# Optimization experiments

Measured on AMD Instinct MI355X. Metric: run time of the kernel, lower is better.

The kernel has to match this reference:

```python
import jax, jax.numpy as jnp
import numpy as np

B, N, K, CIN, COUT, H = 4, 2048, 32, 16, 32, 32
EPS = 1e-5


def setup_inputs() -> dict:
    key = jax.random.key(0)
    ks = jax.random.split(key, 6)
    s = 0.1
    return dict(
        xyz=jax.random.uniform(ks[0], (B, N, 3), dtype=jnp.float32),
        points=jax.random.normal(ks[1], (B, N, CIN), dtype=jnp.float32),
        W1=jax.random.normal(ks[2], (3, H), dtype=jnp.float32) * s,
        b1=jnp.zeros((H,), jnp.float32),
        g1=jnp.ones((H,), jnp.float32),
        be1=jnp.zeros((H,), jnp.float32),
        W2=jax.random.normal(ks[3], (H, H), dtype=jnp.float32) * s,
        b2=jnp.zeros((H,), jnp.float32),
        g2=jnp.ones((H,), jnp.float32),
        be2=jnp.zeros((H,), jnp.float32),
        W3=jax.random.normal(ks[4], (H, CIN * COUT), dtype=jnp.float32) * s,
        b3=jnp.zeros((CIN * COUT,), jnp.float32),
        gbn=jnp.ones((COUT,), jnp.float32),
        bbn=jnp.zeros((COUT,), jnp.float32),
    )


def _bn(h, g, b):
    # BatchNorm1d training-mode math: biased batch stats over axis 0
    return g * (h - h.mean(0)) / jnp.sqrt(h.var(0) + EPS) + b


def reference(xyz, points, W1, b1, g1, be1, W2, b2, g2, be2, W3, b3, gbn, bbn):
    # KNN: squared distances (B,N,N)
    sq = jnp.sum(xyz * xyz, -1)
    dist = -2.0 * jnp.einsum('bmc,bnc->bmn', xyz, xyz) + sq[:, :, None] + sq[:, None, :]
    _, idx = jax.lax.top_k(-dist, K)  # (B,N,K) nearest neighbors

    gather = jax.vmap(lambda p, i: p[i])  # (N,C),(N,K)->(N,K,C), vmapped over B
    grouped_xyz = gather(xyz, idx)                      # (B,N,K,3)
    rel = grouped_xyz - xyz[:, :, None, :]              # (B,N,K,3)
    grouped_pts = gather(points, idx)                   # (B,N,K,CIN)

    # weight net on relative coords
    h = rel.reshape(-1, 3)
    h = _bn(jax.nn.relu(h @ W1 + b1), g1, be1)
    h = _bn(jax.nn.relu(h @ W2 + b2), g2, be2)
    w = (h @ W3 + b3).reshape(B, N, K, CIN, COUT)       # (B,N,K,CIN,COUT)

    # weighted sum over C_in, then max over neighbors
    out = jnp.einsum('bnkc,bnkco->bnko', grouped_pts, w)  # (B,N,K,COUT)
    out = out.max(axis=2)                                 # (B,N,COUT)

    # final BatchNorm1d over (B,N) per channel
    m = out.mean((0, 1))
    v = out.var((0, 1))
    return gbn * (out - m) / jnp.sqrt(v + EPS) + bbn
```

## Files before the change

### kernel.cpp

```cpp
#include <hip/hip_runtime.h>

#define B_ 4
#define N_ 2048
#define K_ 32
#define CIN_ 16
#define COUT_ 32
#define H_ 32
#define R_ (B_*N_*K_)
#define EPS_ 1e-5f
#define INVR_ (1.0f/(float)R_)
#define INVBN_ (1.0f/(float)(B_*N_))
#define LISTCAP 160
#define NSH 16

typedef __attribute__((ext_vector_type(8)))  _Float16 f16x8;
typedef __attribute__((ext_vector_type(2)))  __fp16   hw16x2;
typedef __attribute__((ext_vector_type(2)))  _Float16 f16x2;
typedef __attribute__((ext_vector_type(16))) float    f32x16;

__device__ __forceinline__ float dot3f(float ax,float ay,float az,float bx,float by,float bz){
    return fmaf(az,bz, fmaf(ay,by, ax*bx));
}
__device__ __forceinline__ unsigned int pk2(float a, float b){
    union { hw16x2 v; unsigned int u; } c;
    c.v = __builtin_amdgcn_cvt_pkrtz(a, b);
    return c.u;
}
__device__ __forceinline__ unsigned int pkmul(unsigned int a, unsigned int b){
    union { unsigned int u; f16x2 v; } x, y, r;
    x.u = a; y.u = b; r.v = x.v * y.v; return r.u;
}
__device__ __forceinline__ float shsum(const float* __restrict__ p, int k){
    float s = 0.f;
    #pragma unroll
    for (int i = 0; i < NSH; ++i) s += p[i*32 + k];
    return s;
}

__global__ __launch_bounds__(256) void k_prep0(const float* __restrict__ xyz, const float* __restrict__ points,
                                               float4* __restrict__ xs4g, unsigned int* __restrict__ pf16,
                                               float* __restrict__ st){
    int flat = blockIdx.x*256 + threadIdx.x;
    if (flat < 8192){
        float x = xyz[3*flat], y = xyz[3*flat+1], z = xyz[3*flat+2];
        xs4g[flat] = make_float4(x, y, z, dot3f(x,y,z,x,y,z));
    } else {
        int p = flat - 8192;
        pf16[p] = pk2(points[2*p], points[2*p+1]);
    }
    if (blockIdx.x == 0){
        for (int j = threadIdx.x; j < 1280; j += 256) st[j] = 0.f;
    }
}

__global__ __launch_bounds__(256,7) void k_knn(const float4* __restrict__ xs4g,
                                               const float* __restrict__ W1, const float* __restrict__ b1,
                                               int* __restrict__ idx_out,
                                               float* __restrict__ s1sh, float* __restrict__ q1sh,
                                               unsigned int* __restrict__ h1f){
    __shared__ unsigned int hist[4][512][2];
    __shared__ unsigned long long lst[4][LISTCAP];
    __shared__ int kidx[4][K_];

    const int tid  = threadIdx.x;
    const int w    = tid >> 6;
    const int lane = tid & 63;
    const int half = lane >> 5;
    const int b    = blockIdx.x >> 9;
    const int q    = ((blockIdx.x & 511) << 2) + w;
    const int bN   = b * N_;
    unsigned int* hw = &hist[w][0][0];

    const uint4 z4 = make_uint4(0,0,0,0);
    uint4* h4 = (uint4*)hw;
    #pragma unroll
    for (int i = 0; i < 4; ++i) h4[i*64 + lane] = z4;

    const float4 qp = xs4g[bN + q];
    const float qx = qp.x, qy = qp.y, qz = qp.z, sqq = qp.w;

    #pragma unroll 4
    for (int j = 0; j < 32; ++j){
        int c = j*64 + lane;
        float4 pt = xs4g[bN + c];
        float d = fmaf(-2.0f, dot3f(qx,qy,qz, pt.x,pt.y,pt.z), sqq) + pt.w;
        unsigned int u1 = __float_as_uint(d + 1.0f);
        unsigned int key = (u1 <= 0x3F800000u) ? 0u : ((u1 - 0x3F800000u) >> 15);
        key = key > 511u ? 511u : key;
        atomicAdd(&hw[key*2 + (lane & 1)], 1u);
    }

    unsigned int g[8];
    #pragma unroll
    for (int t = 0; t < 4; ++t){
        uint4 h = ((const uint4*)hw)[lane*4 + t];
        g[2*t]   = h.x + h.y;
        g[2*t+1] = h.z + h.w;
    }
    unsigned int gs = 0;
    #pragma unroll
    for (int t = 0; t < 8; ++t) gs += g[t];
    unsigned int cum = gs;
    #pragma unroll
    for (int off = 1; off < 64; off <<= 1){
        unsigned int v = __shfl_up(cum, off);
        if (lane >= off) cum += v;
    }
    unsigned long long bal = __ballot(cum >= (unsigned)K_);
    int L = __ffsll(bal) - 1;
    unsigned int run = __shfl(cum, L) - __shfl(gs, L);
    int Bsel = 8*L + 7;
    {
        unsigned int c = run; bool fnd = false;
        #pragma unroll
        for (int t = 0; t < 8; ++t){
            unsigned int ht = __shfl(g[t], L, 64);
            if (!fnd && c + ht >= (unsigned)K_){ Bsel = 8*L + t; fnd = true; }
            c += ht;
        }
    }
    const float Tedge = __uint_as_float(0x3F800000u + ((unsigned)(Bsel + 1) << 15));
    const bool allin = (Bsel == 511);

    const unsigned long long mlt = (lane == 63) ? ~0ull >> 1 : (1ull << lane) - 1ull;
    unsigned int cnt = 0;
    #pragma unroll 4
    for (int j = 0; j < 32; ++j){
        int c = j*64 + lane;
        float4 pt = xs4g[bN + c];
        float d = fmaf(-2.0f, dot3f(qx,qy,qz, pt.x,pt.y,pt.z), sqq) + pt.w;
        float f1 = d + 1.0f;
        bool surv = (f1 < Tedge) || allin;
        unsigned long long sb = __ballot(surv);
        unsigned int pos = cnt + (unsigned int)__popcll(sb & mlt);
        if (surv && pos < (unsigned)LISTCAP)
            lst[w][pos] = ((unsigned long long)__float_as_uint(d) << 32) | (unsigned int)c;
        cnt += (unsigned int)__popcll(sb);
    }
    int m = (int)cnt; if (m > LISTCAP) m = LISTCAP;

    int* outp = idx_out + ((size_t)bN + q) * K_;
    for (int i = lane; i < m; i += 64){
        unsigned long long my = lst[w][i];
        int rank = 0;
        for (int jj = 0; jj < m; ++jj)
            rank += (lst[w][jj] < my) ? 1 : 0;
        if (rank < K_){
            int id = (int)(unsigned int)(my & 0xFFFFFFFFull);
            outp[rank] = id;
            kidx[w][rank] = id;
        }
    }

    {
        const int ch = lane & 31;
        float w1a = W1[ch], w1b = W1[H_+ch], w1c = W1[2*H_+ch], b1c = b1[ch];
        float s = 0.f, qq = 0.f;
        #pragma unroll
        for (int r = 0; r < 16; ++r){
            int idr = kidx[w][half*16 + r];
            float4 pn = xs4g[bN + idr];
            float rx = pn.x - qx, ry = pn.y - qy, rz = pn.z - qz;
            float h = fmaxf(fmaf(rx, w1a, fmaf(ry, w1b, fmaf(rz, w1c, b1c))), 0.0f);
            s += h; qq = fmaf(h, h, qq);
        }
        s  += __shfl_xor(s, 32, 64);
        qq += __shfl_xor(qq, 32, 64);
        if (lane < 32){
            int sh = (blockIdx.x & (NSH-1)) * 32 + ch;
            atomicAdd(&s1sh[sh], s);
            atomicAdd(&q1sh[sh], qq);
        }
    }

    {
        const int id = kidx[w][lane & 31];
        float4 pn = xs4g[bN + id];
        float rx = pn.x - qx, ry = pn.y - qy, rz = pn.z - qz;
        uint4* dst = (uint4*)h1f + (size_t)(bN + q)*128 + lane;
        const int c0 = half*8;
        #pragma unroll
        for (int sblk = 0; sblk < 2; ++sblk){
            const int cb = sblk*16 + c0;
            const float4 wa0 = *(const float4*)(W1 + cb);
            const float4 wa1 = *(const float4*)(W1 + cb + 4);
            const float4 wb0 = *(const float4*)(W1 + H_ + cb);
            const float4 wb1 = *(const float4*)(W1 + H_ + cb + 4);
            const float4 wc0 = *(const float4*)(W1 + 2*H_ + cb);
            const float4 wc1 = *(const float4*)(W1 + 2*H_ + cb + 4);
            const float4 bv0 = *(const float4*)(b1 + cb);
            const float4 bv1 = *(const float4*)(b1 + cb + 4);
            float h0 = fmaxf(fmaf(rx, wa0.x, fmaf(ry, wb0.x, fmaf(rz, wc0.x, bv0.x))), 0.0f);
            float h1v= fmaxf(fmaf(rx, wa0.y, fmaf(ry, wb0.y, fmaf(rz, wc0.y, bv0.y))), 0.0f);
            float h2v= fmaxf(fmaf(rx, wa0.z, fmaf(ry, wb0.z, fmaf(rz, wc0.z, bv0.z))), 0.0f);
            float h3 = fmaxf(fmaf(rx, wa0.w, fmaf(ry, wb0.w, fmaf(rz, wc0.w, bv0.w))), 0.0f);
            float h4 = fmaxf(fmaf(rx, wa1.x, fmaf(ry, wb1.x, fmaf(rz, wc1.x, bv1.x))), 0.0f);
            float h5 = fmaxf(fmaf(rx, wa1.y, fmaf(ry, wb1.y, fmaf(rz, wc1.y, bv1.y))), 0.0f);
            float h6 = fmaxf(fmaf(rx, wa1.z, fmaf(ry, wb1.z, fmaf(rz, wc1.z, bv1.z))), 0.0f);
            float h7 = fmaxf(fmaf(rx, wa1.w, fmaf(ry, wb1.w, fmaf(rz, wc1.w, bv1.w))), 0.0f);
            uint4 o;
            o.x = pk2(h0, h1v); o.y = pk2(h2v, h3); o.z = pk2(h4, h5); o.w = pk2(h6, h7);
            dst[sblk*64] = o;
        }
    }
}

__global__ __launch_bounds__(256) void k_prep2(const float* __restrict__ s1s, const float* __restrict__ q1s,
                                               const float* __restrict__ g1, const float* __restrict__ be1,
                                               const float* __restrict__ W2, const float* __restrict__ b2,
                                               unsigned int* __restrict__ W2f, float* __restrict__ b2p){
    int flat = blockIdx.x*256 + threadIdx.x;
    if (flat < 512){
        int d = flat;
        int jj = d & 3, lane = (d >> 2) & 63, s = d >> 8;
        int col = lane & 31;
        int k0 = s*16 + (lane >> 5)*8 + 2*jj;
        float m0 = shsum(s1s,k0)*INVR_,   v0 = shsum(q1s,k0)*INVR_   - m0*m0;
        float m1 = shsum(s1s,k0+1)*INVR_, v1 = shsum(q1s,k0+1)*INVR_ - m1*m1;
        float a0  = g1[k0]   / sqrtf(v0 + EPS_);
        float a1v = g1[k0+1] / sqrtf(v1 + EPS_);
        W2f[d] = pk2(a0*W2[k0*H_ + col], a1v*W2[(k0+1)*H_ + col]);
    } else if (flat < 544){
        int col = flat - 512;
        float acc = b2[col];
        #pragma unroll 4
        for (int h = 0; h < H_; ++h){
            float mm = shsum(s1s,h)*INVR_, vv = shsum(q1s,h)*INVR_ - mm*mm;
            float aa = g1[h] / sqrtf(vv + EPS_);
            float bb = fmaf(-aa, mm, be1[h]);
            acc = fmaf(bb, W2[h*H_ + col], acc);
        }
        b2p[col] = acc;
    }
}

__global__ __launch_bounds__(256,4) void k_h2stats(const uint4* __restrict__ h1f,
                                                   const uint4* __restrict__ W2f, const float* __restrict__ b2p,
                                                   float* gsum, float* gsq){
    __shared__ float redS[H_], redQ[H_];
    const int tid = threadIdx.x, lane = tid & 63, w = tid >> 6;
    const int m = lane & 31;
    if (tid < H_){ redS[tid] = 0.f; redQ[tid] = 0.f; }
    __syncthreads();

    union { uint4 u4; f16x8 v; } Bf0, Bf1;
    Bf0.u4 = W2f[lane];
    Bf1.u4 = W2f[64 + lane];
    float b2c = b2p[m];
    const int blk0 = blockIdx.x*16 + w*4;

    float s = 0.f, q = 0.f;
    #pragma unroll
    for (int t = 0; t < 4; ++t){
        union { uint4 u4; f16x8 v; } a0, a1f;
        a0.u4  = h1f[(size_t)(blk0 + t)*128 + lane];
        a1f.u4 = h1f[(size_t)(blk0 + t)*128 + 64 + lane];
        f32x16 acc;
        #pragma unroll
        for (int i = 0; i < 16; ++i) acc[i] = b2c;
        acc = __builtin_amdgcn_mfma_f32_32x32x16_f16(a0.v,  Bf0.v, acc, 0, 0, 0);
        acc = __builtin_amdgcn_mfma_f32_32x32x16_f16(a1f.v, Bf1.v, acc, 0, 0, 0);
        #pragma unroll
        for (int i = 0; i < 16; ++i){
            float v = fmaxf(acc[i], 0.0f);
            s += v; q = fmaf(v, v, q);
        }
    }
    s += __shfl_xor(s, 32, 64);
    q += __shfl_xor(q, 32, 64);
    if (lane < 32){ atomicAdd(&redS[m], s); atomicAdd(&redQ[m], q); }
    __syncthreads();
    if (tid < H_){ atomicAdd(&gsum[tid], redS[tid]); atomicAdd(&gsq[tid], redQ[tid]); }
}

__global__ __launch_bounds__(256) void k_prep3(const float* __restrict__ W3, const float* __restrict__ b3,
                                               const float* __restrict__ s2, const float* __restrict__ q2,
                                               const float* __restrict__ g2, const float* __restrict__ be2,
                                               unsigned int* __restrict__ W3f){
    int d = blockIdx.x*256 + threadIdx.x;
    int jj = d & 3, lane = (d >> 2) & 63, step = d >> 8;
    int col = lane & 31;
    int off = (lane >> 5)*8 + 2*jj;
    float v0, v1;
    if (step < 32){
        int h = step, c0 = off;
        float mm = s2[h]*INVR_, vv = q2[h]*INVR_ - mm*mm;
        float aa = g2[h] / sqrtf(vv + EPS_);
        v0 = aa * W3[h*512 + c0*COUT_ + col];
        v1 = aa * W3[h*512 + (c0+1)*COUT_ + col];
    } else {
        int c0 = off;
        v0 = b3[c0*COUT_ + col]; v1 = b3[(c0+1)*COUT_ + col];
        #pragma unroll 4
        for (int h = 0; h < H_; ++h){
            float mm = s2[h]*INVR_, vv = q2[h]*INVR_ - mm*mm;
            float aa = g2[h] / sqrtf(vv + EPS_);
            float bb = fmaf(-aa, mm, be2[h]);
            v0 = fmaf(bb, W3[h*512 + c0*COUT_ + col], v0);
            v1 = fmaf(bb, W3[h*512 + (c0+1)*COUT_ + col], v1);
        }
    }
    W3f[d] = pk2(v0, v1);
}

#define PHASEA(T, H2P, GSEL) do { \
    union { uint4 u4; f16x8 v; } B0f, B1f; \
    B0f.u4 = h1f[(size_t)(blk0 + (T))*128 + lane]; \
    B1f.u4 = h1f[(size_t)(blk0 + (T))*128 + 64 + lane]; \
    int row = rB + (T)*32 + m; \
    int bb_ = row >> 16; \
    int idr = idx[row]; \
    const uint4* gpp = (const uint4*)(pf16 + ((size_t)bb_*N_ + idr)*8); \
    uint4 ga = gpp[0], gb = gpp[1]; \
    GSEL[0] = half ? gb.x : ga.x; \
    GSEL[1] = half ? gb.y : ga.y; \
    GSEL[2] = half ? gb.z : ga.z; \
    GSEL[3] = half ? gb.w : ga.w; \
    f32x16 c2; \
    _Pragma("unroll") \
    for (int i = 0; i < 16; ++i) c2[i] = b2v[i]; \
    c2 = __builtin_amdgcn_mfma_f32_32x32x16_f16(A0.v, B0f.v, c2, 0, 0, 0); \
    c2 = __builtin_amdgcn_mfma_f32_32x32x16_f16(A1.v, B1f.v, c2, 0, 0, 0); \
    _Pragma("unroll") \
    for (int p = 0; p < 8; ++p){ \
        float v0 = fmaxf(c2[2*p],   0.0f); \
        float v1 = fmaxf(c2[2*p+1], 0.0f); \
        unsigned int ow = pk2(v0, v1); \
        unsigned int ot = __shfl_xor(ow, 32, 64); \
        int a = p >> 1, bb = p & 1; \
        H2P[4*a + bb]     = half ? ot : ow; \
        H2P[4*a + 2 + bb] = half ? ow : ot; \
    } \
} while(0)

#define REDST(ACC, T) do { \
    float v = ACC[0]; \
    _Pragma("unroll") \
    for (int i = 1; i < 16; ++i) v = fmaxf(v, ACC[i]); \
    v = fmaxf(v, __shfl_xor(v, 32, 64)); \
    if (lane < 32){ \
        int g = blk0 + (T); \
        out_pre[(size_t)g*COUT_ + m] = v; \
        atomicAdd(&redS[m], v); \
        atomicAdd(&redQ[m], v*v); \
    } \
} while(0)

__global__ __launch_bounds__(256,4) void k_out(const uint4* __restrict__ h1f, const int* __restrict__ idx,
                                               const uint4* __restrict__ W2f, const float* __restrict__ b2p,
                                               const unsigned int* __restrict__ pf16,
                                               const uint4* __restrict__ W3f,
                                               float* __restrict__ out_pre, float* gsum, float* gsq){
    __shared__ uint4 Wls[2112];
    __shared__ float redS[COUT_], redQ[COUT_];
    const int tid = threadIdx.x, lane = tid & 63, w = tid >> 6;
    const int half = lane >> 5, m = lane & 31;
    for (int i = tid; i < 2112; i += 256) Wls[i] = W3f[i];
    if (tid < COUT_){ redS[tid] = 0.f; redQ[tid] = 0.f; }
    __syncthreads();

    const int rB = blockIdx.x*256 + w*64;
    const int blk0 = blockIdx.x*8 + w*2;

    union { uint4 u4; f16x8 v; } A0, A1;
    A0.u4 = W2f[lane];
    A1.u4 = W2f[64 + lane];
    float b2v[16];
    #pragma unroll
    for (int i = 0; i < 16; ++i) b2v[i] = b2p[(i&3) + 8*(i>>2) + 4*half];

    unsigned int h2p0[16], h2p1[16];
    unsigned int gsel0[4], gsel1[4];
    PHASEA(0, h2p0, gsel0);
    PHASEA(1, h2p1, gsel1);

    f32x16 acc0, acc1;
    #pragma unroll
    for (int i = 0; i < 16; ++i){ acc0[i] = 0.f; acc1[i] = 0.f; }
    #pragma unroll
    for (int kb = 0; kb < 32; ++kb){
        union { uint4 u4; f16x8 v; } bf; bf.u4 = Wls[kb*64 + lane];
        const unsigned int sel = (kb & 1) ? 0x03020302u : 0x01000100u;
        unsigned int hr0 = h2p0[kb >> 1];
        unsigned int hd0 = __builtin_amdgcn_perm(hr0, hr0, sel);
        union { unsigned int u[4]; f16x8 v; } af;
        #pragma unroll
        for (int jj = 0; jj < 4; ++jj) af.u[jj] = pkmul(hd0, gsel0[jj]);
        acc0 = __builtin_amdgcn_mfma_f32_32x32x16_f16(af.v, bf.v, acc0, 0, 0, 0);
        unsigned int hr1 = h2p1[kb >> 1];
        unsigned int hd1 = __builtin_amdgcn_perm(hr1, hr1, sel);
        #pragma unroll
        for (int jj = 0; jj < 4; ++jj) af.u[jj] = pkmul(hd1, gsel1[jj]);
        acc1 = __builtin_amdgcn_mfma_f32_32x32x16_f16(af.v, bf.v, acc1, 0, 0, 0);
    }
    {
        union { uint4 u4; f16x8 v; } bf; bf.u4 = Wls[32*64 + lane];
        union { unsigned int u[4]; f16x8 v; } af;
        #pragma unroll
        for (int jj = 0; jj < 4; ++jj) af.u[jj] = gsel0[jj];
        acc0 = __builtin_amdgcn_mfma_f32_32x32x16_f16(af.v, bf.v, acc0, 0, 0, 0);
        #pragma unroll
        for (int jj = 0; jj < 4; ++jj) af.u[jj] = gsel1[jj];
        acc1 = __builtin_amdgcn_mfma_f32_32x32x16_f16(af.v, bf.v, acc1, 0, 0, 0);
    }

    REDST(acc0, 0);
    REDST(acc1, 1);

    __syncthreads();
    if (tid < COUT_){ atomicAdd(&gsum[tid], redS[tid]); atomicAdd(&gsq[tid], redQ[tid]); }
}

__global__ __launch_bounds__(256) void k_bn(const float4* __restrict__ out_pre4,
                                            const float* __restrict__ s3, const float* __restrict__ q3,
                                            const float* __restrict__ gbn, const float* __restrict__ bbn,
                                            float4* __restrict__ out4){
    int i = blockIdx.x*256 + threadIdx.x;
    int o = (i*4) & (COUT_-1);
    float4 v = out_pre4[i];
    float4 r;
    {
        float mm = s3[o]*INVBN_;   float vv = q3[o]*INVBN_   - mm*mm;
        float aa = gbn[o]/sqrtf(vv+EPS_);   r.x = fmaf(aa, v.x, fmaf(-aa, mm, bbn[o]));
    }
    {
        float mm = s3[o+1]*INVBN_; float vv = q3[o+1]*INVBN_ - mm*mm;
        float aa = gbn[o+1]/sqrtf(vv+EPS_); r.y = fmaf(aa, v.y, fmaf(-aa, mm, bbn[o+1]));
    }
    {
        float mm = s3[o+2]*INVBN_; float vv = q3[o+2]*INVBN_ - mm*mm;
        float aa = gbn[o+2]/sqrtf(vv+EPS_); r.z = fmaf(aa, v.z, fmaf(-aa, mm, bbn[o+2]));
    }
    {
        float mm = s3[o+3]*INVBN_; float vv = q3[o+3]*INVBN_ - mm*mm;
        float aa = gbn[o+3]/sqrtf(vv+EPS_); r.w = fmaf(aa, v.w, fmaf(-aa, mm, bbn[o+3]));
    }
    out4[i] = r;
}

extern "C" void kernel_launch(void* const* d_in, const int* in_sizes, int n_in,
                              void* d_out, int out_size, void* d_ws, size_t ws_size,
                              hipStream_t stream){
    const float* xyz    = (const float*)d_in[0];
    const float* points = (const float*)d_in[1];
    const float* W1  = (const float*)d_in[2];
    const float* b1  = (const float*)d_in[3];
    const float* g1  = (const float*)d_in[4];
    const float* be1 = (const float*)d_in[5];
    const float* W2  = (const float*)d_in[6];
    const float* b2  = (const float*)d_in[7];
    const float* g2  = (const float*)d_in[8];
    const float* be2 = (const float*)d_in[9];
    const float* W3  = (const float*)d_in[10];
    const float* b3  = (const float*)d_in[11];
    const float* gbn = (const float*)d_in[12];
    const float* bbn = (const float*)d_in[13];
    float* out = (float*)d_out;

    char* base = (char*)d_ws;
    int*            idx     = (int*)(base + 0);
    float*          out_pre = (float*)(base + 1048576);
    unsigned int*   pf16    = (unsigned int*)(base + 2097152);
    unsigned int*   W3f     = (unsigned int*)(base + 2359296);
    unsigned int*   W2f     = (unsigned int*)(base + 2393088);
    float*          b2p     = (float*)(base + 2395136);
    float*          st      = (float*)(base + 2395264);
    float4*         xs4g    = (float4*)(base + 2400384);
    unsigned int*   h1f     = (unsigned int*)(base + 4194304);
    float *s1s=st, *q1s=st+512, *s2=st+1024, *q2=st+1056, *s3=st+1088, *q3=st+1120;

    hipLaunchKernelGGL(k_prep0,   dim3(288),      dim3(256), 0, stream, xyz, points, xs4g, pf16, st);
    hipLaunchKernelGGL(k_knn,     dim3(B_*N_/4),  dim3(256), 0, stream, xs4g, W1, b1, idx, s1s, q1s, h1f);
    hipLaunchKernelGGL(k_prep2,   dim3(3),        dim3(256), 0, stream, s1s, q1s, g1, be1, W2, b2, W2f, b2p);
    hipLaunchKernelGGL(k_h2stats, dim3(R_/512),   dim3(256), 0, stream, (const uint4*)h1f,
                       (const uint4*)W2f, b2p, s2, q2);
    hipLaunchKernelGGL(k_prep3,   dim3(33),       dim3(256), 0, stream, W3, b3, s2, q2, g2, be2, W3f);
    hipLaunchKernelGGL(k_out,     dim3(R_/256),   dim3(256), 0, stream, (const uint4*)h1f, idx,
                       (const uint4*)W2f, b2p, pf16, (const uint4*)W3f, out_pre, s3, q3);
    hipLaunchKernelGGL(k_bn,      dim3(256),      dim3(256), 0, stream, (const float4*)out_pre, s3, q3,
                       gbn, bbn, (float4*)out);
}
```

Baseline: 178.7 us.

## Fold weight-prep kernels into consumers and cache KNN distances in registers

The small k_prep2 and k_prep3 kernels are removed. Each block of k_h2stats and k_out now rebuilds the BN-folded W2/b2 (and in k_out the W3/b3 tile) in shared memory from the batch statistics, which saves two launches and their serialization gaps. In exchange every block repeats the fold, including strided W3 global reads and a 32-step bias loop, across 1024 k_out blocks. Separately, k_knn keeps the 32 per-lane distances in registers so the second pass does not recompute them. That pass is now fully unrolled and the occupancy hint drops from 7 to 5 waves to make room for the extra registers.

```diff
diff --git a/kernel.cpp b/kernel.cpp
--- a/kernel.cpp
+++ b/kernel.cpp
@@ -53,7 +53,7 @@
     }
 }
 
-__global__ __launch_bounds__(256,7) void k_knn(const float4* __restrict__ xs4g,
+__global__ __launch_bounds__(256,5) void k_knn(const float4* __restrict__ xs4g,
                                                const float* __restrict__ W1, const float* __restrict__ b1,
                                                int* __restrict__ idx_out,
                                                float* __restrict__ s1sh, float* __restrict__ q1sh,
@@ -79,11 +79,13 @@
     const float4 qp = xs4g[bN + q];
     const float qx = qp.x, qy = qp.y, qz = qp.z, sqq = qp.w;
 
-    #pragma unroll 4
+    unsigned int fv[32];
+    #pragma unroll
     for (int j = 0; j < 32; ++j){
         int c = j*64 + lane;
         float4 pt = xs4g[bN + c];
         float d = fmaf(-2.0f, dot3f(qx,qy,qz, pt.x,pt.y,pt.z), sqq) + pt.w;
+        fv[j] = __float_as_uint(d);
         unsigned int u1 = __float_as_uint(d + 1.0f);
         unsigned int key = (u1 <= 0x3F800000u) ? 0u : ((u1 - 0x3F800000u) >> 15);
         key = key > 511u ? 511u : key;
@@ -124,17 +126,14 @@
 
     const unsigned long long mlt = (lane == 63) ? ~0ull >> 1 : (1ull << lane) - 1ull;
     unsigned int cnt = 0;
-    #pragma unroll 4
+    #pragma unroll
     for (int j = 0; j < 32; ++j){
-        int c = j*64 + lane;
-        float4 pt = xs4g[bN + c];
-        float d = fmaf(-2.0f, dot3f(qx,qy,qz, pt.x,pt.y,pt.z), sqq) + pt.w;
-        float f1 = d + 1.0f;
+        float f1 = __uint_as_float(fv[j]) + 1.0f;
         bool surv = (f1 < Tedge) || allin;
         unsigned long long sb = __ballot(surv);
         unsigned int pos = cnt + (unsigned int)__popcll(sb & mlt);
         if (surv && pos < (unsigned)LISTCAP)
-            lst[w][pos] = ((unsigned long long)__float_as_uint(d) << 32) | (unsigned int)c;
+            lst[w][pos] = ((unsigned long long)fv[j] << 32) | (unsigned int)(j*64 + lane);
         cnt += (unsigned int)__popcll(sb);
     }
     int m = (int)cnt; if (m > LISTCAP) m = LISTCAP;
@@ -205,48 +204,53 @@
     }
 }
 
-__global__ __launch_bounds__(256) void k_prep2(const float* __restrict__ s1s, const float* __restrict__ q1s,
-                                               const float* __restrict__ g1, const float* __restrict__ be1,
-                                               const float* __restrict__ W2, const float* __restrict__ b2,
-                                               unsigned int* __restrict__ W2f, float* __restrict__ b2p){
-    int flat = blockIdx.x*256 + threadIdx.x;
-    if (flat < 512){
-        int d = flat;
-        int jj = d & 3, lane = (d >> 2) & 63, s = d >> 8;
-        int col = lane & 31;
-        int k0 = s*16 + (lane >> 5)*8 + 2*jj;
-        float m0 = shsum(s1s,k0)*INVR_,   v0 = shsum(q1s,k0)*INVR_   - m0*m0;
-        float m1 = shsum(s1s,k0+1)*INVR_, v1 = shsum(q1s,k0+1)*INVR_ - m1*m1;
-        float a0  = g1[k0]   / sqrtf(v0 + EPS_);
-        float a1v = g1[k0+1] / sqrtf(v1 + EPS_);
-        W2f[d] = pk2(a0*W2[k0*H_ + col], a1v*W2[(k0+1)*H_ + col]);
-    } else if (flat < 544){
-        int col = flat - 512;
-        float acc = b2[col];
+__device__ __forceinline__ void build_l2(const float* __restrict__ s1s, const float* __restrict__ q1s,
+                                         const float* __restrict__ g1, const float* __restrict__ be1,
+                                         const float* __restrict__ W2, const float* __restrict__ b2,
+                                         float* a1L, float* bb1L, unsigned int* W2L, float* b2pL,
+                                         int tid){
+    if (tid < H_){
+        float s = shsum(s1s, tid), qq = shsum(q1s, tid);
+        float mm = s*INVR_, vv = qq*INVR_ - mm*mm;
+        float aa = g1[tid] / sqrtf(vv + EPS_);
+        a1L[tid]  = aa;
+        bb1L[tid] = fmaf(-aa, mm, be1[tid]);
+    }
+    __syncthreads();
+    #pragma unroll
+    for (int e = 0; e < 2; ++e){
+        int d = tid*2 + e;
+        int jj = d & 3, ln = (d >> 2) & 63, s = d >> 8;
+        int col = ln & 31;
+        int k0 = s*16 + ((ln >> 5) << 3) + 2*jj;
+        W2L[d] = pk2(a1L[k0]*W2[k0*H_ + col], a1L[k0+1]*W2[(k0+1)*H_ + col]);
+    }
+    if (tid < H_){
+        float acc = b2[tid];
         #pragma unroll 4
-        for (int h = 0; h < H_; ++h){
-            float mm = shsum(s1s,h)*INVR_, vv = shsum(q1s,h)*INVR_ - mm*mm;
-            float aa = g1[h] / sqrtf(vv + EPS_);
-            float bb = fmaf(-aa, mm, be1[h]);
-            acc = fmaf(bb, W2[h*H_ + col], acc);
-        }
-        b2p[col] = acc;
+        for (int h = 0; h < H_; ++h) acc = fmaf(bb1L[h], W2[h*H_ + tid], acc);
+        b2pL[tid] = acc;
     }
 }
 
 __global__ __launch_bounds__(256,4) void k_h2stats(const uint4* __restrict__ h1f,
-                                                   const uint4* __restrict__ W2f, const float* __restrict__ b2p,
+                                                   const float* __restrict__ s1s, const float* __restrict__ q1s,
+                                                   const float* __restrict__ g1, const float* __restrict__ be1,
+                                                   const float* __restrict__ W2, const float* __restrict__ b2,
                                                    float* gsum, float* gsq){
     __shared__ float redS[H_], redQ[H_];
+    __shared__ float a1L[H_], bb1L[H_], b2pL[H_];
+    __shared__ unsigned int W2L[512];
     const int tid = threadIdx.x, lane = tid & 63, w = tid >> 6;
     const int m = lane & 31;
     if (tid < H_){ redS[tid] = 0.f; redQ[tid] = 0.f; }
+    build_l2(s1s, q1s, g1, be1, W2, b2, a1L, bb1L, W2L, b2pL, tid);
     __syncthreads();
 
     union { uint4 u4; f16x8 v; } Bf0, Bf1;
-    Bf0.u4 = W2f[lane];
-    Bf1.u4 = W2f[64 + lane];
-    float b2c = b2p[m];
+    Bf0.u4 = ((const uint4*)W2L)[lane];
+    Bf1.u4 = ((const uint4*)W2L)[64 + lane];
+    float b2c = b2pL[m];
     const int blk0 = blockIdx.x*16 + w*4;
 
     float s = 0.f, q = 0.f;
@@ -271,36 +275,6 @@
     if (lane < 32){ atomicAdd(&redS[m], s); atomicAdd(&redQ[m], q); }
     __syncthreads();
     if (tid < H_){ atomicAdd(&gsum[tid], redS[tid]); atomicAdd(&gsq[tid], redQ[tid]); }
-}
-
-__global__ __launch_bounds__(256) void k_prep3(const float* __restrict__ W3, const float* __restrict__ b3,
-                                               const float* __restrict__ s2, const float* __restrict__ q2,
-                                               const float* __restrict__ g2, const float* __restrict__ be2,
-                                               unsigned int* __restrict__ W3f){
-    int d = blockIdx.x*256 + threadIdx.x;
-    int jj = d & 3, lane = (d >> 2) & 63, step = d >> 8;
-    int col = lane & 31;
-    int off = (lane >> 5)*8 + 2*jj;
-    float v0, v1;
-    if (step < 32){
-        int h = step, c0 = off;
-        float mm = s2[h]*INVR_, vv = q2[h]*INVR_ - mm*mm;
-        float aa = g2[h] / sqrtf(vv + EPS_);
-        v0 = aa * W3[h*512 + c0*COUT_ + col];
-        v1 = aa * W3[h*512 + (c0+1)*COUT_ + col];
-    } else {
-        int c0 = off;
-        v0 = b3[c0*COUT_ + col]; v1 = b3[(c0+1)*COUT_ + col];
-        #pragma unroll 4
-        for (int h = 0; h < H_; ++h){
-            float mm = s2[h]*INVR_, vv = q2[h]*INVR_ - mm*mm;
-            float aa = g2[h] / sqrtf(vv + EPS_);
-            float bb = fmaf(-aa, mm, be2[h]);
-            v0 = fmaf(bb, W3[h*512 + c0*COUT_ + col], v0);
-            v1 = fmaf(bb, W3[h*512 + (c0+1)*COUT_ + col], v1);
-        }
-    }
-    W3f[d] = pk2(v0, v1);
 }
 
 #define PHASEA(T, H2P, GSEL) do { \
@@ -347,27 +321,56 @@
 } while(0)
 
 __global__ __launch_bounds__(256,4) void k_out(const uint4* __restrict__ h1f, const int* __restrict__ idx,
-                                               const uint4* __restrict__ W2f, const float* __restrict__ b2p,
+                                               const float* __restrict__ s1s, const float* __restrict__ q1s,
+                                               const float* __restrict__ g1, const float* __restrict__ be1,
+                                               const float* __restrict__ W2, const float* __restrict__ b2,
+                                               const float* __restrict__ s2, const float* __restrict__ q2,
+                                               const float* __restrict__ g2, const float* __restrict__ be2,
+                                               const float* __restrict__ W3, const float* __restrict__ b3,
                                                const unsigned int* __restrict__ pf16,
-                                               const uint4* __restrict__ W3f,
                                                float* __restrict__ out_pre, float* gsum, float* gsq){
     __shared__ uint4 Wls[2112];
     __shared__ float redS[COUT_], redQ[COUT_];
+    __shared__ float a1L[H_], bb1L[H_], b2pL[H_], aa2L[H_], bb2L[H_];
+    __shared__ unsigned int W2L[512];
     const int tid = threadIdx.x, lane = tid & 63, w = tid >> 6;
     const int half = lane >> 5, m = lane & 31;
-    for (int i = tid; i < 2112; i += 256) Wls[i] = W3f[i];
-    if (tid < COUT_){ redS[tid] = 0.f; redQ[tid] = 0.f; }
+    if (tid < COUT_){
+        redS[tid] = 0.f; redQ[tid] = 0.f;
+        float mm = s2[tid]*INVR_, vv = q2[tid]*INVR_ - mm*mm;
+        float aa = g2[tid] / sqrtf(vv + EPS_);
+        aa2L[tid] = aa;
+        bb2L[tid] = fmaf(-aa, mm, be2[tid]);
+    }
+    build_l2(s1s, q1s, g1, be1, W2, b2, a1L, bb1L, W2L, b2pL, tid);
+    {
+        int jj = tid & 3, ln = tid >> 2;
+        int col = ln & 31, c0 = ((ln >> 5) << 3) + 2*jj;
+        unsigned int* WlsD = (unsigned int*)Wls;
+        #pragma unroll 4
+        for (int i = 0; i < 32; ++i){
+            float a = aa2L[i];
+            WlsD[i*256 + tid] = pk2(a*W3[i*512 + c0*COUT_ + col], a*W3[i*512 + (c0+1)*COUT_ + col]);
+        }
+        float v0 = b3[c0*COUT_ + col], v1 = b3[(c0+1)*COUT_ + col];
+        #pragma unroll 4
+        for (int h = 0; h < H_; ++h){
+            v0 = fmaf(bb2L[h], W3[h*512 + c0*COUT_ + col], v0);
+            v1 = fmaf(bb2L[h], W3[h*512 + (c0+1)*COUT_ + col], v1);
+        }
+        WlsD[32*256 + tid] = pk2(v0, v1);
+    }
     __syncthreads();
 
     const int rB = blockIdx.x*256 + w*64;
     const int blk0 = blockIdx.x*8 + w*2;
 
     union { uint4 u4; f16x8 v; } A0, A1;
-    A0.u4 = W2f[lane];
-    A1.u4 = W2f[64 + lane];
+    A0.u4 = ((const uint4*)W2L)[lane];
+    A1.u4 = ((const uint4*)W2L)[64 + lane];
     float b2v[16];
     #pragma unroll
-    for (int i = 0; i < 16; ++i) b2v[i] = b2p[(i&3) + 8*(i>>2) + 4*half];
+    for (int i = 0; i < 16; ++i) b2v[i] = b2pL[(i&3) + 8*(i>>2) + 4*half];
 
     unsigned int h2p0[16], h2p1[16];
     unsigned int gsel0[4], gsel1[4];
@@ -461,9 +464,6 @@
     int*            idx     = (int*)(base + 0);
     float*          out_pre = (float*)(base + 1048576);
     unsigned int*   pf16    = (unsigned int*)(base + 2097152);
-    unsigned int*   W3f     = (unsigned int*)(base + 2359296);
-    unsigned int*   W2f     = (unsigned int*)(base + 2393088);
-    float*          b2p     = (float*)(base + 2395136);
     float*          st      = (float*)(base + 2395264);
     float4*         xs4g    = (float4*)(base + 2400384);
     unsigned int*   h1f     = (unsigned int*)(base + 4194304);
@@ -471,12 +471,10 @@
 
     hipLaunchKernelGGL(k_prep0,   dim3(288),      dim3(256), 0, stream, xyz, points, xs4g, pf16, st);
     hipLaunchKernelGGL(k_knn,     dim3(B_*N_/4),  dim3(256), 0, stream, xs4g, W1, b1, idx, s1s, q1s, h1f);
-    hipLaunchKernelGGL(k_prep2,   dim3(3),        dim3(256), 0, stream, s1s, q1s, g1, be1, W2, b2, W2f, b2p);
     hipLaunchKernelGGL(k_h2stats, dim3(R_/512),   dim3(256), 0, stream, (const uint4*)h1f,
-                       (const uint4*)W2f, b2p, s2, q2);
-    hipLaunchKernelGGL(k_prep3,   dim3(33),       dim3(256), 0, stream, W3, b3, s2, q2, g2, be2, W3f);
+                       s1s, q1s, g1, be1, W2, b2, s2, q2);
     hipLaunchKernelGGL(k_out,     dim3(R_/256),   dim3(256), 0, stream, (const uint4*)h1f, idx,
-                       (const uint4*)W2f, b2p, pf16, (const uint4*)W3f, out_pre, s3, q3);
+                       s1s, q1s, g1, be1, W2, b2, s2, q2, g2, be2, W3, b3, pf16, out_pre, s3, q3);
     hipLaunchKernelGGL(k_bn,      dim3(256),      dim3(256), 0, stream, (const float4*)out_pre, s3, q3,
                        gbn, bbn, (float4*)out);
 }
```

Result: faster. 169.8 us (-5.0%).
